# Optimization experiments

Measured on AMD Instinct MI355X. Metric: run time of the kernel, lower is better.

Reference implementation:

```python
import jax, jax.numpy as jnp
import numpy as np
from jax import lax

KS = 21        # kernel_size
FS = 32        # sampling frequency: grid = linspace(0, KS/FS, KS)
FEATURES = 3   # = input channels (depthwise Gaussian)
CHUNK = 2304   # lax.map batch_size over flattened pixels (6912 = 3 chunks)
L = 1.0        # self.l


def gaussian_kernels(gamma):
    """Per-feature isotropic Gaussian taps, energy-normalized. -> (KS,KS,1,F) HWIO depthwise."""
    x = jnp.linspace(0.0, KS / FS, KS)
    xx, yy = jnp.meshgrid(x, x)
    mean = KS / (2.0 * FS)
    sigma = 1.0 / gamma                      # (F,)
    r2 = (xx - mean) ** 2 + (yy - mean) ** 2  # (KS,KS)
    amp = (FS ** 2) / (2.0 * jnp.pi * sigma ** 2)
    k = amp * jnp.exp(-r2[..., None] / (2.0 * sigma ** 2))   # (KS,KS,F)
    # normalize_energy=True: unit L2 energy per feature
    k = k / jnp.sqrt((k ** 2).sum(axis=(0, 1), keepdims=True))
    return k[:, :, None, :]


def gauss_conv(x, gamma):
    """Depthwise Gaussian blur, NHWC, SAME padding, stride 1."""
    k = gaussian_kernels(gamma).astype(x.dtype)
    return lax.conv_general_dilated(
        x, k, window_strides=(1, 1), padding='SAME',
        dimension_numbers=('NHWC', 'HWIO', 'NHWC'),
        feature_group_count=x.shape[-1])


def setup_inputs() -> dict:
    key = jax.random.key(0)
    k1, k2, k3, k4 = jax.random.split(key, 4)
    inputs = jax.random.uniform(k1, (4, 48, 48, 3), dtype=jnp.float32)
    gamma_m = jax.random.uniform(k2, (FEATURES,), jnp.float32, 0.2, 2.0)
    gamma_w = jax.random.uniform(k3, (FEATURES,), jnp.float32, 0.2, 2.0)
    gamma_g = jax.random.uniform(k4, (FEATURES,), jnp.float32, 0.2, 2.0)
    return {"inputs": inputs, "gamma_m": gamma_m, "gamma_w": gamma_w, "gamma_g": gamma_g}


def _per_image_diffs(img, blur):
    """For each scalar pixel x of img: mean over ALL of blur of tanh(x - blur)."""
    bf = blur.reshape(-1)                     # (Nb,)
    flat = img.reshape(-1)                    # (N,)
    chunks = flat.reshape(-1, CHUNK)          # (N/CHUNK, CHUNK)

    def f(ch):  # (CHUNK,) -> (CHUNK,)  ; tile is (CHUNK, Nb)
        return jnp.tanh(ch[:, None] - bf[None, :]).mean(axis=-1)

    return lax.map(f, chunks).reshape(img.shape)


def _inrf(inputs, gamma_m, gamma_w, gamma_g):
    first_term = gauss_conv(inputs, gamma_m)          # M(inputs)
    blurred = gauss_conv(inputs, gamma_g)             # G(inputs)
    # sequential over batch (mirrors lax.scan over leading axis)
    difference = lax.map(lambda t: _per_image_diffs(t[0], t[1]), (inputs, blurred))
    second_term = gauss_conv(difference, gamma_w)     # W(difference)
    return first_term - L * second_term


def reference(inputs, gamma_m, gamma_w, gamma_g):
    return _inrf(inputs, gamma_m, gamma_w, gamma_g)
```

## Files before the change

### kernel.cpp

```cpp
#include <hip/hip_runtime.h>

#define KS   21
#define HH   48
#define WW   48
#define CC   3
#define ROW  (WW*CC)
#define NB   4
#define NPIX (HH*WW*CC)
#define NTOT (NB*NPIX)
#define TPB  256
#define NBLK (NTOT/TPB)
#define SEGS (NPIX/TPB)
#define CTAN 2.8853900817779268f
#define B_HI 5.0f
#define B_LO -4.0f

__device__ __forceinline__ float fast_exp2(float x) {
#if __has_builtin(__builtin_amdgcn_exp2f)
    return __builtin_amdgcn_exp2f(x);
#else
    return __expf(x * 0.6931471805599453f);
#endif
}
__device__ __forceinline__ float fast_rcp(float x) {
#if __has_builtin(__builtin_amdgcn_rcpf)
    return __builtin_amdgcn_rcpf(x);
#else
    return 1.0f / x;
#endif
}

__device__ __forceinline__ float tap1d(const float* g, int f, int i) {
    float sigma  = 1.0f / g[f];
    float inv2s2 = 0.5f / (sigma * sigma);
    const float step = 21.0f / 640.0f, mean = 21.0f / 64.0f;
    float r = (float)i * step - mean;
    float v = expf(-r * r * inv2s2);
    float ss = 0.0f;
    for (int j = 0; j < KS; ++j) {
        float rj = (float)j * step - mean;
        float vj = expf(-rj * rj * inv2s2);
        ss += vj * vj;
    }
    return v * rsqrtf(ss);
}

__global__ __launch_bounds__(TPB) void hconv_mg(
    const float* __restrict__ in, const float* __restrict__ gm,
    const float* __restrict__ gg, float* __restrict__ hm, float* __restrict__ hg)
{
    __shared__ float sm[63], sg[63];
    const int t = threadIdx.x;
    if (t < 126) {
        int set = t / 63, f = (t % 63) / 21, i = t % 21;
        float v = tap1d(set ? gg : gm, f, i);
        (set ? sg : sm)[t % 63] = v;
    }
    __syncthreads();
    const int idx = blockIdx.x * TPB + t;
    const int c = idx % CC, w = (idx / CC) % WW;
    const int rowstart = idx - w * CC;
    float tm[KS], tg[KS];
#pragma unroll
    for (int k = 0; k < KS; ++k) { tm[k] = sm[c * 21 + k]; tg[k] = sg[c * 21 + k]; }
    float am = 0.f, ag = 0.f;
#pragma unroll
    for (int k = 0; k < KS; ++k) {
        int wc = w + k - 10;
        int wcc = min(max(wc, 0), WW - 1);
        float v = in[rowstart + wcc * CC];
        bool ok = (unsigned)wc < (unsigned)WW;
        am = fmaf(v, ok ? tm[k] : 0.f, am);
        ag = fmaf(v, ok ? tg[k] : 0.f, ag);
    }
    hm[idx] = am;
    hg[idx] = ag;
}

__global__ __launch_bounds__(TPB) void vconv_mg(
    const float* __restrict__ hm, const float* __restrict__ hg,
    const float* __restrict__ gm, const float* __restrict__ gg,
    float* __restrict__ first, float* __restrict__ active,
    int* __restrict__ segcnt, int* __restrict__ netcnt,
    float* __restrict__ diffsum)
{
    __shared__ float sm[63], sg[63];
    __shared__ int wcnt[4], wnet[4];
    const int t = threadIdx.x;
    if (t < 126) {
        int set = t / 63, f = (t % 63) / 21, i = t % 21;
        float v = tap1d(set ? gg : gm, f, i);
        (set ? sg : sm)[t % 63] = v;
    }
    __syncthreads();
    const int idx = blockIdx.x * TPB + t;
    const int c = idx % CC, h = (idx / ROW) % HH;
    const int n = blockIdx.x / SEGS, seg = blockIdx.x % SEGS;
    float tm[KS], tg[KS];
#pragma unroll
    for (int k = 0; k < KS; ++k) { tm[k] = sm[c * 21 + k]; tg[k] = sg[c * 21 + k]; }
    float am = 0.f, ag = 0.f;
#pragma unroll
    for (int k = 0; k < KS; ++k) {
        int hc = h + k - 10;
        int hcc = min(max(hc, 0), HH - 1);
        int off = idx + (hcc - h) * ROW;
        bool ok = (unsigned)hc < (unsigned)HH;
        am = fmaf(hm[off], ok ? tm[k] : 0.f, am);
        ag = fmaf(hg[off], ok ? tg[k] : 0.f, ag);
    }
    first[idx] = am;
    diffsum[idx] = 0.0f;

    const float b = ag;
    const bool satpos = (b <= B_LO);
    const bool satneg = (b >= B_HI);
    const bool act = !(satpos || satneg);
    const int lane = t & 63, wid = t >> 6;
    unsigned long long mb = __ballot(act);
    int cnt = __popcll(mb);
    int netc = __popcll(__ballot(satpos)) - __popcll(__ballot(satneg));
    if (lane == 0) { wcnt[wid] = cnt; wnet[wid] = netc; }
    __syncthreads();
    int pre = 0;
    for (int j = 0; j < wid; ++j) pre += wcnt[j];
    if (act) {
        int pos = pre + __popcll(mb & ((1ull << lane) - 1ull));
        active[n * NPIX + seg * TPB + pos] = CTAN * b;
    }
    if (t == 0) {
        segcnt[blockIdx.x] = wcnt[0] + wcnt[1] + wcnt[2] + wcnt[3];
        netcnt[blockIdx.x] = wnet[0] + wnet[1] + wnet[2] + wnet[3];
    }
}

__global__ __launch_bounds__(TPB) void diff_kernel(
    const float* __restrict__ in, const float* __restrict__ active,
    const int* __restrict__ segcnt, float* __restrict__ diffsum)
{
    const int n = blockIdx.y, seg = blockIdx.z;
    const int len = segcnt[n * SEGS + seg];
    if (len == 0) return;
    __shared__ float sb[TPB];
    const int t = threadIdx.x;
    if (t < len) sb[t] = active[n * NPIX + seg * TPB + t];
    __syncthreads();
    const int p = blockIdx.x * TPB + t;
    float cx = CTAN * in[n * NPIX + p];
    float acc = 0.0f;
#pragma unroll 4
    for (int q = 0; q < len; ++q)
        acc += fast_rcp(fast_exp2(cx - sb[q]) + 1.0f);
    atomicAdd(&diffsum[n * NPIX + p], (float)len - 2.0f * acc);
}

__global__ __launch_bounds__(TPB) void hconv_w(
    const float* __restrict__ diffsum, const float* __restrict__ gw,
    const int* __restrict__ netcnt, float* __restrict__ tmp)
{
    __shared__ float sw[63];
    const int t = threadIdx.x;
    if (t < 63) sw[t] = tap1d(gw, t / 21, t % 21);
    __syncthreads();
    const int idx = blockIdx.x * TPB + t;
    const int c = idx % CC, w = (idx / CC) % WW;
    const int n = blockIdx.x / SEGS;
    float netf = 0.f;
    for (int s = 0; s < SEGS; ++s) netf += (float)netcnt[n * SEGS + s];
    const int rowstart = idx - w * CC;
    float tw[KS];
#pragma unroll
    for (int k = 0; k < KS; ++k) tw[k] = sw[c * 21 + k];
    float a = 0.f;
#pragma unroll
    for (int k = 0; k < KS; ++k) {
        int wc = w + k - 10;
        int wcc = min(max(wc, 0), WW - 1);
        float v = diffsum[rowstart + wcc * CC] + netf;
        bool ok = (unsigned)wc < (unsigned)WW;
        a = fmaf(v, ok ? tw[k] : 0.f, a);
    }
    tmp[idx] = a * (1.0f / (float)NPIX);
}

__global__ __launch_bounds__(TPB) void vconv_w_sub(
    const float* __restrict__ tmp, const float* __restrict__ gw,
    const float* __restrict__ first, float* __restrict__ out)
{
    __shared__ float sw[63];
    const int t = threadIdx.x;
    if (t < 63) sw[t] = tap1d(gw, t / 21, t % 21);
    __syncthreads();
    const int idx = blockIdx.x * TPB + t;
    const int c = idx % CC, h = (idx / ROW) % HH;
    float tw[KS];
#pragma unroll
    for (int k = 0; k < KS; ++k) tw[k] = sw[c * 21 + k];
    float a = 0.f;
#pragma unroll
    for (int k = 0; k < KS; ++k) {
        int hc = h + k - 10;
        int hcc = min(max(hc, 0), HH - 1);
        bool ok = (unsigned)hc < (unsigned)HH;
        a = fmaf(tmp[idx + (hcc - h) * ROW], ok ? tw[k] : 0.f, a);
    }
    out[idx] = first[idx] - a;
}

extern "C" void kernel_launch(void* const* d_in, const int* in_sizes, int n_in,
                              void* d_out, int out_size, void* d_ws, size_t ws_size,
                              hipStream_t stream) {
    const float* in = (const float*)d_in[0];
    const float* gm = (const float*)d_in[1];
    const float* gw = (const float*)d_in[2];
    const float* gg = (const float*)d_in[3];
    float* out = (float*)d_out;

    float* wsf     = (float*)d_ws;
    float* hm      = wsf;
    float* hg      = hm + NTOT;
    float* first   = hg + NTOT;
    float* active  = first + NTOT;
    float* diffsum = active + NTOT;
    float* tmp     = diffsum + NTOT;
    int*   segcnt  = (int*)(tmp + NTOT);
    int*   netcnt  = segcnt + NBLK;

    hconv_mg<<<NBLK, TPB, 0, stream>>>(in, gm, gg, hm, hg);
    vconv_mg<<<NBLK, TPB, 0, stream>>>(hm, hg, gm, gg, first, active, segcnt, netcnt, diffsum);
    diff_kernel<<<dim3(SEGS, NB, SEGS), TPB, 0, stream>>>(in, active, segcnt, diffsum);
    hconv_w<<<NBLK, TPB, 0, stream>>>(diffsum, gw, netcnt, tmp);
    vconv_w_sub<<<NBLK, TPB, 0, stream>>>(tmp, gw, first, out);
}
```

Measured before the change: 78.50 us.

## Fuse all five stages into one cooperative kernel with grid syncs

Replaces the five separate launches with a single cooperative kernel of 108 blocks that separates the stages with grid.sync(). The diff stage now has each thread loop over all active segments itself, rather than spreading the work over a 3D grid with atomics. The aim is to remove per-launch overhead and the atomics. The cost is far less parallelism in the tanh-pair stage: about 27k threads each walk up to 2304 entries, where before the work was split across 3888 blocks. Grid syncs also add their own latency.

```diff
diff --git a/kernel.cpp b/kernel.cpp
--- a/kernel.cpp
+++ b/kernel.cpp
@@ -1,4 +1,7 @@
 #include <hip/hip_runtime.h>
+#include <hip/hip_cooperative_groups.h>
+
+namespace cg = cooperative_groups;
 
 #define KS   21
 #define HH   48
@@ -45,166 +48,145 @@
     return v * rsqrtf(ss);
 }
 
-__global__ __launch_bounds__(TPB) void hconv_mg(
+__global__ __launch_bounds__(TPB) void inrf_all(
     const float* __restrict__ in, const float* __restrict__ gm,
-    const float* __restrict__ gg, float* __restrict__ hm, float* __restrict__ hg)
+    const float* __restrict__ gw, const float* __restrict__ gg,
+    float* __restrict__ hm, float* __restrict__ hg,
+    float* __restrict__ diffsum, float* __restrict__ tmp,
+    float* __restrict__ active, int* __restrict__ segcnt,
+    int* __restrict__ netcnt, float* __restrict__ out)
 {
-    __shared__ float sm[63], sg[63];
-    const int t = threadIdx.x;
-    if (t < 126) {
+    cg::grid_group grid = cg::this_grid();
+    __shared__ float st[192];
+    __shared__ float sb[TPB];
+    __shared__ int wcnt[4], wnet[4];
+
+    const int t   = threadIdx.x;
+    const int blk = blockIdx.x;
+    const int idx = blk * TPB + t;
+    const int n   = blk / SEGS;
+    const int seg = blk % SEGS;
+    const int r   = idx % NPIX;
+    const int c   = r % CC;
+    const int w   = (r / CC) % WW;
+    const int h   = r / ROW;
+
+    if (t < 189) {
         int set = t / 63, f = (t % 63) / 21, i = t % 21;
-        float v = tap1d(set ? gg : gm, f, i);
-        (set ? sg : sm)[t % 63] = v;
+        const float* g = (set == 0) ? gm : (set == 1) ? gg : gw;
+        st[t] = tap1d(g, f, i);
     }
     __syncthreads();
-    const int idx = blockIdx.x * TPB + t;
-    const int c = idx % CC, w = (idx / CC) % WW;
-    const int rowstart = idx - w * CC;
-    float tm[KS], tg[KS];
-#pragma unroll
-    for (int k = 0; k < KS; ++k) { tm[k] = sm[c * 21 + k]; tg[k] = sg[c * 21 + k]; }
-    float am = 0.f, ag = 0.f;
-#pragma unroll
-    for (int k = 0; k < KS; ++k) {
-        int wc = w + k - 10;
-        int wcc = min(max(wc, 0), WW - 1);
-        float v = in[rowstart + wcc * CC];
-        bool ok = (unsigned)wc < (unsigned)WW;
-        am = fmaf(v, ok ? tm[k] : 0.f, am);
-        ag = fmaf(v, ok ? tg[k] : 0.f, ag);
-    }
-    hm[idx] = am;
-    hg[idx] = ag;
-}
-
-__global__ __launch_bounds__(TPB) void vconv_mg(
-    const float* __restrict__ hm, const float* __restrict__ hg,
-    const float* __restrict__ gm, const float* __restrict__ gg,
-    float* __restrict__ first, float* __restrict__ active,
-    int* __restrict__ segcnt, int* __restrict__ netcnt,
-    float* __restrict__ diffsum)
-{
-    __shared__ float sm[63], sg[63];
-    __shared__ int wcnt[4], wnet[4];
-    const int t = threadIdx.x;
-    if (t < 126) {
-        int set = t / 63, f = (t % 63) / 21, i = t % 21;
-        float v = tap1d(set ? gg : gm, f, i);
-        (set ? sg : sm)[t % 63] = v;
-    }
-    __syncthreads();
-    const int idx = blockIdx.x * TPB + t;
-    const int c = idx % CC, h = (idx / ROW) % HH;
-    const int n = blockIdx.x / SEGS, seg = blockIdx.x % SEGS;
-    float tm[KS], tg[KS];
-#pragma unroll
-    for (int k = 0; k < KS; ++k) { tm[k] = sm[c * 21 + k]; tg[k] = sg[c * 21 + k]; }
-    float am = 0.f, ag = 0.f;
-#pragma unroll
-    for (int k = 0; k < KS; ++k) {
-        int hc = h + k - 10;
-        int hcc = min(max(hc, 0), HH - 1);
-        int off = idx + (hcc - h) * ROW;
-        bool ok = (unsigned)hc < (unsigned)HH;
-        am = fmaf(hm[off], ok ? tm[k] : 0.f, am);
-        ag = fmaf(hg[off], ok ? tg[k] : 0.f, ag);
-    }
-    first[idx] = am;
-    diffsum[idx] = 0.0f;
-
-    const float b = ag;
-    const bool satpos = (b <= B_LO);
-    const bool satneg = (b >= B_HI);
-    const bool act = !(satpos || satneg);
-    const int lane = t & 63, wid = t >> 6;
-    unsigned long long mb = __ballot(act);
-    int cnt = __popcll(mb);
-    int netc = __popcll(__ballot(satpos)) - __popcll(__ballot(satneg));
-    if (lane == 0) { wcnt[wid] = cnt; wnet[wid] = netc; }
-    __syncthreads();
-    int pre = 0;
-    for (int j = 0; j < wid; ++j) pre += wcnt[j];
-    if (act) {
-        int pos = pre + __popcll(mb & ((1ull << lane) - 1ull));
-        active[n * NPIX + seg * TPB + pos] = CTAN * b;
-    }
-    if (t == 0) {
-        segcnt[blockIdx.x] = wcnt[0] + wcnt[1] + wcnt[2] + wcnt[3];
-        netcnt[blockIdx.x] = wnet[0] + wnet[1] + wnet[2] + wnet[3];
-    }
-}
-
-__global__ __launch_bounds__(TPB) void diff_kernel(
-    const float* __restrict__ in, const float* __restrict__ active,
-    const int* __restrict__ segcnt, float* __restrict__ diffsum)
-{
-    const int n = blockIdx.y, seg = blockIdx.z;
-    const int len = segcnt[n * SEGS + seg];
-    if (len == 0) return;
-    __shared__ float sb[TPB];
-    const int t = threadIdx.x;
-    if (t < len) sb[t] = active[n * NPIX + seg * TPB + t];
-    __syncthreads();
-    const int p = blockIdx.x * TPB + t;
-    float cx = CTAN * in[n * NPIX + p];
-    float acc = 0.0f;
-#pragma unroll 4
-    for (int q = 0; q < len; ++q)
-        acc += fast_rcp(fast_exp2(cx - sb[q]) + 1.0f);
-    atomicAdd(&diffsum[n * NPIX + p], (float)len - 2.0f * acc);
-}
-
-__global__ __launch_bounds__(TPB) void hconv_w(
-    const float* __restrict__ diffsum, const float* __restrict__ gw,
-    const int* __restrict__ netcnt, float* __restrict__ tmp)
-{
-    __shared__ float sw[63];
-    const int t = threadIdx.x;
-    if (t < 63) sw[t] = tap1d(gw, t / 21, t % 21);
-    __syncthreads();
-    const int idx = blockIdx.x * TPB + t;
-    const int c = idx % CC, w = (idx / CC) % WW;
-    const int n = blockIdx.x / SEGS;
-    float netf = 0.f;
-    for (int s = 0; s < SEGS; ++s) netf += (float)netcnt[n * SEGS + s];
-    const int rowstart = idx - w * CC;
-    float tw[KS];
-#pragma unroll
-    for (int k = 0; k < KS; ++k) tw[k] = sw[c * 21 + k];
-    float a = 0.f;
-#pragma unroll
-    for (int k = 0; k < KS; ++k) {
-        int wc = w + k - 10;
-        int wcc = min(max(wc, 0), WW - 1);
-        float v = diffsum[rowstart + wcc * CC] + netf;
-        bool ok = (unsigned)wc < (unsigned)WW;
-        a = fmaf(v, ok ? tw[k] : 0.f, a);
-    }
-    tmp[idx] = a * (1.0f / (float)NPIX);
-}
-
-__global__ __launch_bounds__(TPB) void vconv_w_sub(
-    const float* __restrict__ tmp, const float* __restrict__ gw,
-    const float* __restrict__ first, float* __restrict__ out)
-{
-    __shared__ float sw[63];
-    const int t = threadIdx.x;
-    if (t < 63) sw[t] = tap1d(gw, t / 21, t % 21);
-    __syncthreads();
-    const int idx = blockIdx.x * TPB + t;
-    const int c = idx % CC, h = (idx / ROW) % HH;
-    float tw[KS];
-#pragma unroll
-    for (int k = 0; k < KS; ++k) tw[k] = sw[c * 21 + k];
-    float a = 0.f;
-#pragma unroll
-    for (int k = 0; k < KS; ++k) {
-        int hc = h + k - 10;
-        int hcc = min(max(hc, 0), HH - 1);
-        bool ok = (unsigned)hc < (unsigned)HH;
-        a = fmaf(tmp[idx + (hcc - h) * ROW], ok ? tw[k] : 0.f, a);
-    }
-    out[idx] = first[idx] - a;
+
+    {
+        const int rowstart = idx - w * CC;
+        float am = 0.f, ag = 0.f;
+#pragma unroll
+        for (int k = 0; k < KS; ++k) {
+            int wc  = w + k - 10;
+            int wcc = min(max(wc, 0), WW - 1);
+            float v = in[rowstart + wcc * CC];
+            bool ok = (unsigned)wc < (unsigned)WW;
+            am = fmaf(v, ok ? st[c * 21 + k]      : 0.f, am);
+            ag = fmaf(v, ok ? st[63 + c * 21 + k] : 0.f, ag);
+        }
+        hm[idx] = am; hg[idx] = ag;
+    }
+    __threadfence();
+    grid.sync();
+
+    float firstv;
+    {
+        float am = 0.f, ag = 0.f;
+#pragma unroll
+        for (int k = 0; k < KS; ++k) {
+            int hc  = h + k - 10;
+            int hcc = min(max(hc, 0), HH - 1);
+            int off = idx + (hcc - h) * ROW;
+            bool ok = (unsigned)hc < (unsigned)HH;
+            am = fmaf(hm[off], ok ? st[c * 21 + k]      : 0.f, am);
+            ag = fmaf(hg[off], ok ? st[63 + c * 21 + k] : 0.f, ag);
+        }
+        firstv = am;
+        const float b = ag;
+        const bool satpos = (b <= B_LO);
+        const bool satneg = (b >= B_HI);
+        const bool act = !(satpos || satneg);
+        const int lane = t & 63, wid = t >> 6;
+        unsigned long long mb_act = __ballot(act);
+        unsigned long long mb_pos = __ballot(satpos);
+        unsigned long long mb_neg = __ballot(satneg);
+        if (lane == 0) {
+            wcnt[wid] = __popcll(mb_act);
+            wnet[wid] = __popcll(mb_pos) - __popcll(mb_neg);
+        }
+        __syncthreads();
+        int pre = 0;
+        for (int j = 0; j < wid; ++j) pre += wcnt[j];
+        if (act) {
+            int pos = pre + __popcll(mb_act & ((1ull << lane) - 1ull));
+            active[n * NPIX + seg * TPB + pos] = CTAN * b;
+        }
+        if (t == 0) {
+            segcnt[blk] = wcnt[0] + wcnt[1] + wcnt[2] + wcnt[3];
+            netcnt[blk] = wnet[0] + wnet[1] + wnet[2] + wnet[3];
+        }
+    }
+    __threadfence();
+    grid.sync();
+
+    {
+        const float cx = CTAN * in[idx];
+        float acc0 = 0.f, acc1 = 0.f;
+        int lensum = 0, net = 0;
+        for (int s = 0; s < SEGS; ++s) {
+            int len = segcnt[n * SEGS + s];
+            net += netcnt[n * SEGS + s];
+            if (len) {
+                __syncthreads();
+                if (t < len) sb[t] = active[n * NPIX + s * TPB + t];
+                __syncthreads();
+                lensum += len;
+                int q = 0;
+                for (; q + 1 < len; q += 2) {
+                    acc0 += fast_rcp(fast_exp2(cx - sb[q]) + 1.0f);
+                    acc1 += fast_rcp(fast_exp2(cx - sb[q + 1]) + 1.0f);
+                }
+                if (q < len) acc0 += fast_rcp(fast_exp2(cx - sb[q]) + 1.0f);
+            }
+        }
+        diffsum[idx] = ((float)(net + lensum) - 2.0f * (acc0 + acc1))
+                       * (1.0f / (float)NPIX);
+    }
+    __threadfence();
+    grid.sync();
+
+    {
+        const int rowstart = idx - w * CC;
+        float a = 0.f;
+#pragma unroll
+        for (int k = 0; k < KS; ++k) {
+            int wc  = w + k - 10;
+            int wcc = min(max(wc, 0), WW - 1);
+            bool ok = (unsigned)wc < (unsigned)WW;
+            a = fmaf(diffsum[rowstart + wcc * CC], ok ? st[126 + c * 21 + k] : 0.f, a);
+        }
+        tmp[idx] = a;
+    }
+    __threadfence();
+    grid.sync();
+
+    {
+        float a = 0.f;
+#pragma unroll
+        for (int k = 0; k < KS; ++k) {
+            int hc  = h + k - 10;
+            int hcc = min(max(hc, 0), HH - 1);
+            bool ok = (unsigned)hc < (unsigned)HH;
+            a = fmaf(tmp[idx + (hcc - h) * ROW], ok ? st[126 + c * 21 + k] : 0.f, a);
+        }
+        out[idx] = firstv - a;
+    }
 }
 
 extern "C" void kernel_launch(void* const* d_in, const int* in_sizes, int n_in,
@@ -219,16 +201,15 @@
     float* wsf     = (float*)d_ws;
     float* hm      = wsf;
     float* hg      = hm + NTOT;
-    float* first   = hg + NTOT;
-    float* active  = first + NTOT;
-    float* diffsum = active + NTOT;
+    float* diffsum = hg + NTOT;
     float* tmp     = diffsum + NTOT;
-    int*   segcnt  = (int*)(tmp + NTOT);
+    float* active  = tmp + NTOT;
+    int*   segcnt  = (int*)(active + NTOT);
     int*   netcnt  = segcnt + NBLK;
 
-    hconv_mg<<<NBLK, TPB, 0, stream>>>(in, gm, gg, hm, hg);
-    vconv_mg<<<NBLK, TPB, 0, stream>>>(hm, hg, gm, gg, first, active, segcnt, netcnt, diffsum);
-    diff_kernel<<<dim3(SEGS, NB, SEGS), TPB, 0, stream>>>(in, active, segcnt, diffsum);
-    hconv_w<<<NBLK, TPB, 0, stream>>>(diffsum, gw, netcnt, tmp);
-    vconv_w_sub<<<NBLK, TPB, 0, stream>>>(tmp, gw, first, out);
-}
+    void* args[] = { (void*)&in, (void*)&gm, (void*)&gw, (void*)&gg,
+                     (void*)&hm, (void*)&hg, (void*)&diffsum, (void*)&tmp,
+                     (void*)&active, (void*)&segcnt, (void*)&netcnt, (void*)&out };
+    hipLaunchCooperativeKernel((const void*)inrf_all, dim3(NBLK), dim3(TPB),
+                               args, 0, stream);
+}
```

New measurement: 182.6 us. +132.6%, slower.
